# Kernel optimization log

Measured on AMD Instinct MI355X. Metric: run time of the kernel, lower is better.

The kernel has to match this reference:

```python
import jax, jax.numpy as jnp
import numpy as np

B, T, C, HS = 8, 2048, 1024, 128

def setup_inputs() -> dict:
    key = jax.random.key(0)
    kx, kq, kk, kv = jax.random.split(key, 4)
    x = jax.random.normal(kx, (B, T, C), dtype=jnp.float32)
    # torch Linear(C, HS, bias=False): y = x @ W^T with W [HS, C].
    # We store the transposed form [C, HS] and right-multiply (same math).
    scale = 1.0 / np.sqrt(C)  # torch default init scale-ish; exact init irrelevant for correctness
    Wq = jax.random.normal(kq, (C, HS), dtype=jnp.float32) * scale
    Wk = jax.random.normal(kk, (C, HS), dtype=jnp.float32) * scale
    Wv = jax.random.normal(kv, (C, HS), dtype=jnp.float32) * scale
    return {"x": x, "Wq": Wq, "Wk": Wk, "Wv": Wv}

def reference(x, Wq, Wk, Wv):
    Bx, Tx, Cx = x.shape
    q = x @ Wq  # [B, T, HS]
    k = x @ Wk
    v = x @ Wv
    # NOTE: original scales by C**-0.5 where C = n_embd (not head_size)
    wei = jnp.einsum('btd,bsd->bts', q, k) * (Cx ** -0.5)  # [B, T, T]
    causal = jnp.tril(jnp.ones((Tx, Tx), dtype=bool))
    wei = jnp.where(causal, wei, -jnp.inf)
    wei = jax.nn.softmax(wei, axis=-1)
    # dropout rate 0.0 (eval semantics) -> identity
    return jnp.einsum('bts,bsd->btd', wei, v)  # [B, T, HS]
```

## Files before the change

kernel.cpp:

```cpp
#include <hip/hip_runtime.h>
#include <hip/hip_bf16.h>
#include <stdint.h>

typedef float f32x4 __attribute__((ext_vector_type(4)));
typedef float f32x4v __attribute__((ext_vector_type(4)));
typedef short short8 __attribute__((ext_vector_type(8)));
typedef unsigned short u16;
typedef unsigned short u16x8 __attribute__((ext_vector_type(8)));
typedef unsigned short u16x4 __attribute__((ext_vector_type(4)));

#define MFMA16x16x32 __builtin_amdgcn_mfma_f32_16x16x32_bf16

__device__ __forceinline__ u16 f2bf(float f) {
    unsigned int u = __builtin_bit_cast(unsigned int, f);
    u += 0x7fffu + ((u >> 16) & 1u);
    return (u16)(u >> 16);
}

__device__ __forceinline__ void gload_lds16(const void* g, void* l) {
    __builtin_amdgcn_global_load_lds(
        (const __attribute__((address_space(1))) uint32_t*)g,
        (__attribute__((address_space(3))) uint32_t*)l, 16, 0, 0);
}

__device__ __forceinline__ int z_small(int na) {
    int za = (8 * na + 32) / 33;
    return za < 1 ? 1 : za;
}

__global__ void k_transpose_wf(const float* __restrict__ Wq, const float* __restrict__ Wk,
                               const float* __restrict__ Wv, u16* __restrict__ WTf) {
    int tid  = blockIdx.x * 256 + threadIdx.x;
    int f    = tid >> 6;
    int lane = tid & 63;
    int kt  = f / 48;
    int rem = f % 48;
    int ks  = rem / 24;
    int nc  = rem % 24;
    int col = nc * 16 + (lane & 15);
    int w   = col >> 7, n = col & 127;
    int k0  = kt * 64 + ks * 32 + (lane >> 4) * 8;
    const float* W = (w == 0) ? Wq : ((w == 1) ? Wk : Wv);
    u16x8 v;
#pragma unroll
    for (int j = 0; j < 8; ++j)
        v[j] = f2bf(W[(size_t)(k0 + j) * 128 + n]);
    *(u16x8*)(&WTf[(size_t)tid * 8]) = v;
}

__global__ __launch_bounds__(512) void k_qkv_gemm8(
    const float* __restrict__ x, const u16* __restrict__ WTf,
    u16* __restrict__ qb, u16* __restrict__ kb, u16* __restrict__ vT)
{
    __shared__ u16 abuf[2][64 * 64];
    __shared__ u16 bbuf[2][384 * 64];
    const int tid  = threadIdx.x;
    const int lane = tid & 63, wid = tid >> 6;
    const int wr = wid >> 2, wc = wid & 3;
    const int lrow = lane & 15, lk = lane >> 4;
    const int m0 = blockIdx.x * 64;

    const int arow = tid >> 3;
    const int aseg = tid & 7;
    const float* xsrc = x + (size_t)(m0 + arow) * 1024 + aseg * 8;

    f32x4 acc[2][6];
#pragma unroll
    for (int i = 0; i < 2; ++i)
#pragma unroll
        for (int j = 0; j < 6; ++j) acc[i][j] = (f32x4){0.f, 0.f, 0.f, 0.f};

#define LOADA(s0, s1, ktv)                                                     \
    s0 = *(const f32x4v*)(xsrc + (ktv) * 64);                                  \
    s1 = *(const f32x4v*)(xsrc + (ktv) * 64 + 4);

#define STOREA(buf, s0, s1)                                                    \
    {   u16x8 v;                                                               \
        v[0]=f2bf(s0[0]); v[1]=f2bf(s0[1]); v[2]=f2bf(s0[2]); v[3]=f2bf(s0[3]); \
        v[4]=f2bf(s1[0]); v[5]=f2bf(s1[1]); v[6]=f2bf(s1[2]); v[7]=f2bf(s1[3]); \
        *(u16x8*)(&buf[arow * 64 + ((aseg ^ (arow & 7)) << 3)]) = v; }

#define ISSUEB(buf, ktv)                                                       \
    {   const u16* bsrc = WTf + (size_t)(ktv) * 24576;                         \
        _Pragma("unroll") for (int i = 0; i < 6; ++i) {                        \
            int c = tid + i * 512;                                             \
            gload_lds16(bsrc + c * 8, &buf[c * 8]);                            \
        } }

#define COMPUTE(ab, bb)                                                        \
    _Pragma("unroll") for (int ks = 0; ks < 2; ++ks) {                         \
        short8 af[2];                                                          \
        _Pragma("unroll") for (int mf = 0; mf < 2; ++mf) {                     \
            int row = wr * 32 + mf * 16 + lrow;                                \
            int blk = (ks * 4 + lk) ^ (row & 7);                               \
            af[mf] = *(const short8*)(&ab[row * 64 + (blk << 3)]);             \
        }                                                                      \
        _Pragma("unroll") for (int nf = 0; nf < 6; ++nf) {                     \
            short8 bfr = *(const short8*)(&bb[(ks * 24 + wc * 6 + nf) * 512 + lane * 8]); \
            _Pragma("unroll") for (int mf = 0; mf < 2; ++mf)                   \
                acc[mf][nf] = MFMA16x16x32(af[mf], bfr, acc[mf][nf], 0, 0, 0); \
        } }

#define WAITBAR()                                                              \
    asm volatile("s_waitcnt vmcnt(2) lgkmcnt(0)\n\ts_barrier" ::: "memory");   \
    __builtin_amdgcn_sched_barrier(0);

    f32x4v a0A, a1A, a0B, a1B;
    LOADA(a0A, a1A, 0);
    LOADA(a0B, a1B, 1);
    STOREA(abuf[0], a0A, a1A);
    ISSUEB(bbuf[0], 0);
    LOADA(a0A, a1A, 2);
    WAITBAR();

    for (int kt = 0; kt < 16; kt += 2) {
        {
            const int ktn = (kt + 1 < 16) ? kt + 1 : 15;
            ISSUEB(bbuf[1], ktn);
            __builtin_amdgcn_sched_barrier(0);
            COMPUTE(abuf[0], bbuf[0]);
            STOREA(abuf[1], a0B, a1B);
            const int kp = (kt + 3 < 16) ? kt + 3 : 15;
            LOADA(a0B, a1B, kp);
            WAITBAR();
        }
        {
            const int ktn = (kt + 2 < 16) ? kt + 2 : 15;
            ISSUEB(bbuf[0], ktn);
            __builtin_amdgcn_sched_barrier(0);
            COMPUTE(abuf[1], bbuf[1]);
            STOREA(abuf[0], a0A, a1A);
            const int kp = (kt + 4 < 16) ? kt + 4 : 15;
            LOADA(a0A, a1A, kp);
            WAITBAR();
        }
    }
#undef LOADA
#undef STOREA
#undef ISSUEB
#undef COMPUTE
#undef WAITBAR

#pragma unroll
    for (int nf = 0; nf < 6; ++nf) {
        const int gc   = wc * 96 + nf * 16 + lrow;
        const int wsel = gc >> 7;
        const int col  = gc & 127;
#pragma unroll
        for (int mf = 0; mf < 2; ++mf) {
            const int row0 = m0 + wr * 32 + mf * 16 + lk * 4;
            if (wsel == 0) {
#pragma unroll
                for (int jj = 0; jj < 4; ++jj)
                    qb[(size_t)(row0 + jj) * 128 + col] = f2bf(acc[mf][nf][jj]);
            } else if (wsel == 1) {
#pragma unroll
                for (int jj = 0; jj < 4; ++jj)
                    kb[(size_t)(row0 + jj) * 128 + col] = f2bf(acc[mf][nf][jj]);
            } else {
                const int bb = row0 >> 11, t0 = row0 & 2047;
                u16x4 v;
#pragma unroll
                for (int jj = 0; jj < 4; ++jj) v[jj] = f2bf(acc[mf][nf][jj]);
                *(u16x4*)(&vT[((size_t)bb * 128 + col) * 2048 + t0]) = v;
            }
        }
    }
}

__global__ __launch_bounds__(256) void k_flash6(
    const u16* __restrict__ qb, const u16* __restrict__ kb, const u16* __restrict__ vT,
    float* __restrict__ po, float* __restrict__ pm, float* __restrict__ pl)
{
    __shared__ u16 k_lds[64 * 128];
    __shared__ u16 v_lds[128 * 64];
    __shared__ u16 p_lds[4 * 16 * 64];
    const int tid  = threadIdx.x;
    const int lane = tid & 63, wid = tid >> 6;
    const int lrow = lane & 15, lk = lane >> 4;
    const int bx = blockIdx.x;
    const int b  = bx & 7;
    const int p  = (bx >> 3) & 15;
    const int z  = bx >> 7;

    const int na = p + 1;
    const int za = z_small(na);
    int qt, n, k, Z;
    if (z < za) { qt = p;      n = na;     k = z;      Z = za;     }
    else        { qt = 31 - p; n = 32 - p; k = z - za; Z = 8 - za; }
    const int t0 = (k * n) / Z;
    const int t1 = ((k + 1) * n) / Z;

    const int qrow0 = qt * 64;
    short8 qf[4];
    {
        const u16* qp = qb + ((size_t)b * 2048 + qrow0 + wid * 16 + lrow) * 128;
#pragma unroll
        for (int ks = 0; ks < 4; ++ks) qf[ks] = *(const short8*)(qp + ks * 32 + lk * 8);
    }
    f32x4 of[8];
#pragma unroll
    for (int i = 0; i < 8; ++i) of[i] = (f32x4){0.f, 0.f, 0.f, 0.f};
    float mrun[4], lsum[4];
#pragma unroll
    for (int j = 0; j < 4; ++j) { mrun[j] = -1e30f; lsum[j] = 0.f; }

    const u16* kbase = kb + (size_t)b * 2048 * 128;
    const u16* vbase = vT + (size_t)b * 128 * 2048;
    u16* pw = p_lds + wid * (16 * 64);

    for (int t = t0; t < t1; ++t) {
        const int kv0 = t << 6;
        __syncthreads();
#pragma unroll
        for (int i = 0; i < 4; ++i) {
            int c = tid + i * 256;
            int row = c >> 4, blk = c & 15;
            gload_lds16(kbase + (size_t)(kv0 + row) * 128 + ((blk ^ (row & 7)) << 3),
                        &k_lds[c * 8]);
        }
#pragma unroll
        for (int i = 0; i < 4; ++i) {
            int c = tid + i * 256;
            int row = c >> 3, blk = c & 7;
            gload_lds16(vbase + (size_t)row * 2048 + kv0 + ((blk ^ (row & 7)) << 3),
                        &v_lds[c * 8]);
        }
        __syncthreads();

        f32x4 sf[4];
#pragma unroll
        for (int nf = 0; nf < 4; ++nf) sf[nf] = (f32x4){0.f, 0.f, 0.f, 0.f};
#pragma unroll
        for (int ks = 0; ks < 4; ++ks)
#pragma unroll
            for (int nf = 0; nf < 4; ++nf) {
                int row = nf * 16 + lrow;
                int blk = (ks * 4 + lk) ^ (row & 7);
                short8 bfr = *(const short8*)(&k_lds[row * 128 + (blk << 3)]);
                sf[nf] = MFMA16x16x32(qf[ks], bfr, sf[nf], 0, 0, 0);
            }

        const bool diag = (t == n - 1);
#pragma unroll
        for (int nf = 0; nf < 4; ++nf)
#pragma unroll
            for (int jj = 0; jj < 4; ++jj) {
                float s = sf[nf][jj] * 0.03125f;
                if (diag && (nf * 16 + lrow > wid * 16 + lk * 4 + jj)) s = -1e30f;
                sf[nf][jj] = s;
            }
        float mt[4];
#pragma unroll
        for (int jj = 0; jj < 4; ++jj)
            mt[jj] = fmaxf(fmaxf(sf[0][jj], sf[1][jj]), fmaxf(sf[2][jj], sf[3][jj]));
#pragma unroll
        for (int off = 1; off < 16; off <<= 1)
#pragma unroll
            for (int jj = 0; jj < 4; ++jj)
                mt[jj] = fmaxf(mt[jj], __shfl_xor(mt[jj], off));
        bool small = true;
#pragma unroll
        for (int jj = 0; jj < 4; ++jj) small = small && (mt[jj] <= mrun[jj] + 8.f);
        if (!__all(small)) {
#pragma unroll
            for (int jj = 0; jj < 4; ++jj) {
                float mnew = fmaxf(mrun[jj], mt[jj]);
                float sc   = __expf(mrun[jj] - mnew);
                mrun[jj]   = mnew;
                lsum[jj]  *= sc;
#pragma unroll
                for (int df = 0; df < 8; ++df) of[df][jj] *= sc;
            }
        }
        float rs[4] = {0.f, 0.f, 0.f, 0.f};
#pragma unroll
        for (int nf = 0; nf < 4; ++nf)
#pragma unroll
            for (int jj = 0; jj < 4; ++jj) {
                float e = __expf(sf[nf][jj] - mrun[jj]);
                sf[nf][jj] = e;
                rs[jj] += e;
            }
#pragma unroll
        for (int off = 1; off < 16; off <<= 1)
#pragma unroll
            for (int jj = 0; jj < 4; ++jj)
                rs[jj] += __shfl_xor(rs[jj], off);
#pragma unroll
        for (int jj = 0; jj < 4; ++jj) lsum[jj] += rs[jj];

#pragma unroll
        for (int nf = 0; nf < 4; ++nf)
#pragma unroll
            for (int jj = 0; jj < 4; ++jj) {
                int row = lk * 4 + jj;
                int col = nf * 16 + lrow;
                pw[row * 64 + (((col >> 3) ^ (row & 7)) << 3) + (col & 7)] = f2bf(sf[nf][jj]);
            }
        asm volatile("s_waitcnt lgkmcnt(0)" ::: "memory");
        __builtin_amdgcn_sched_barrier(0);
        short8 paf[2];
#pragma unroll
        for (int ks2 = 0; ks2 < 2; ++ks2) {
            int blk = (ks2 * 4 + lk) ^ (lrow & 7);
            paf[ks2] = *(const short8*)(&pw[lrow * 64 + (blk << 3)]);
        }
#pragma unroll
        for (int ks2 = 0; ks2 < 2; ++ks2)
#pragma unroll
            for (int df = 0; df < 8; ++df) {
                int row = df * 16 + lrow;
                int blk = (ks2 * 4 + lk) ^ (row & 7);
                short8 vf = *(const short8*)(&v_lds[row * 64 + (blk << 3)]);
                of[df] = MFMA16x16x32(paf[ks2], vf, of[df], 0, 0, 0);
            }
    }

    float* poslab = po + (size_t)bx * (64 * 128);
#pragma unroll
    for (int df = 0; df < 8; ++df)
#pragma unroll
        for (int jj = 0; jj < 4; ++jj)
            poslab[(size_t)(wid * 16 + lk * 4 + jj) * 128 + df * 16 + lrow] = of[df][jj];
    if (lrow == 0) {
#pragma unroll
        for (int jj = 0; jj < 4; ++jj) {
            pm[(size_t)bx * 64 + wid * 16 + lk * 4 + jj] = mrun[jj];
            pl[(size_t)bx * 64 + wid * 16 + lk * 4 + jj] = lsum[jj];
        }
    }
}

__global__ __launch_bounds__(256) void k_combine(
    const float* __restrict__ po, const float* __restrict__ pm, const float* __restrict__ pl,
    float* __restrict__ out)
{
    const int row  = blockIdx.x * 4 + (threadIdx.x >> 6);
    const int lane = threadIdx.x & 63;
    const int b  = row >> 11;
    const int t  = row & 2047;
    const int qt = t >> 6;
    const int r  = t & 63;

    const int p  = (qt < 16) ? qt : 31 - qt;
    const int za = z_small(p + 1);
    const int zlo = (qt < 16) ? 0 : za;
    const int zhi = (qt < 16) ? za : 8;

    float M = -1e30f;
    for (int z = zlo; z < zhi; ++z)
        M = fmaxf(M, pm[(size_t)(b + 8 * p + 128 * z) * 64 + r]);
    float den = 0.f, a0 = 0.f, a1 = 0.f;
    for (int z = zlo; z < zhi; ++z) {
        const int bxp = b + 8 * p + 128 * z;
        const float w = __expf(pm[(size_t)bxp * 64 + r] - M);
        den += w * pl[(size_t)bxp * 64 + r];
        const float* slab = po + ((size_t)bxp * 64 + r) * 128;
        a0 += w * slab[lane];
        a1 += w * slab[lane + 64];
    }
    const float inv = 1.f / den;
    out[(size_t)row * 128 + lane]      = a0 * inv;
    out[(size_t)row * 128 + lane + 64] = a1 * inv;
}

extern "C" void kernel_launch(void* const* d_in, const int* in_sizes, int n_in,
                              void* d_out, int out_size, void* d_ws, size_t ws_size,
                              hipStream_t stream) {
    const float* x  = (const float*)d_in[0];
    const float* Wq = (const float*)d_in[1];
    const float* Wk = (const float*)d_in[2];
    const float* Wv = (const float*)d_in[3];
    float* out = (float*)d_out;

    char* ws = (char*)d_ws;
    u16*   qb  = (u16*)(ws);
    u16*   kb  = (u16*)(ws + (size_t)4  * 1048576);
    u16*   vT  = (u16*)(ws + (size_t)8  * 1048576);
    u16*   WTf = (u16*)(ws + (size_t)12 * 1048576);
    float* po  = (float*)(ws + (size_t)13 * 1048576);
    float* pm  = (float*)(ws + (size_t)47 * 1048576);
    float* pl  = (float*)(ws + (size_t)48 * 1048576);

    k_transpose_wf<<<192, 256, 0, stream>>>(Wq, Wk, Wv, WTf);
    k_qkv_gemm8<<<256, 512, 0, stream>>>(x, WTf, qb, kb, vT);
    k_flash6<<<1024, 256, 0, stream>>>(qb, kb, vT, po, pm, pl);
    k_combine<<<4096, 256, 0, stream>>>(po, pm, pl, out);
}
```

Baseline: 78.86 us.

## Double-buffer K/V tiles in LDS and prefetch next tile during compute

The flash attention kernel now keeps two LDS buffers for K and V. It issues the async global-to-LDS loads for the next KV tile right after a single barrier, then computes on the current tile. This overlaps global memory latency with MFMA work and cuts the two barriers per iteration down to one. The cost is double the K/V LDS footprint, which may lower occupancy.

```diff
diff --git a/kernel.cpp b/kernel.cpp
--- a/kernel.cpp
+++ b/kernel.cpp
@@ -168,12 +168,12 @@
     }
 }
 
-__global__ __launch_bounds__(256) void k_flash6(
+__global__ __launch_bounds__(256) void k_flash7(
     const u16* __restrict__ qb, const u16* __restrict__ kb, const u16* __restrict__ vT,
     float* __restrict__ po, float* __restrict__ pm, float* __restrict__ pl)
 {
-    __shared__ u16 k_lds[64 * 128];
-    __shared__ u16 v_lds[128 * 64];
+    __shared__ u16 k_lds[2][64 * 128];
+    __shared__ u16 v_lds[2][128 * 64];
     __shared__ u16 p_lds[4 * 16 * 64];
     const int tid  = threadIdx.x;
     const int lane = tid & 63, wid = tid >> 6;
@@ -209,24 +209,29 @@
     const u16* vbase = vT + (size_t)b * 128 * 2048;
     u16* pw = p_lds + wid * (16 * 64);
 
+#define ISSUE_KV(c_, t_)                                                       \
+    {   const int kv0_ = (t_) << 6;                                            \
+        _Pragma("unroll") for (int i = 0; i < 4; ++i) {                        \
+            int ch = tid + i * 256;                                            \
+            int row = ch >> 4, blk = ch & 15;                                  \
+            gload_lds16(kbase + (size_t)(kv0_ + row) * 128 + ((blk ^ (row & 7)) << 3), \
+                        &k_lds[c_][ch * 8]);                                   \
+        }                                                                      \
+        _Pragma("unroll") for (int i = 0; i < 4; ++i) {                        \
+            int ch = tid + i * 256;                                            \
+            int row = ch >> 3, blk = ch & 7;                                   \
+            gload_lds16(vbase + (size_t)row * 2048 + kv0_ + ((blk ^ (row & 7)) << 3), \
+                        &v_lds[c_][ch * 8]);                                   \
+        }                                                                      \
+        __builtin_amdgcn_sched_barrier(0); }
+
+    ISSUE_KV(0, t0);
+    int c = 0;
+
     for (int t = t0; t < t1; ++t) {
-        const int kv0 = t << 6;
-        __syncthreads();
-#pragma unroll
-        for (int i = 0; i < 4; ++i) {
-            int c = tid + i * 256;
-            int row = c >> 4, blk = c & 15;
-            gload_lds16(kbase + (size_t)(kv0 + row) * 128 + ((blk ^ (row & 7)) << 3),
-                        &k_lds[c * 8]);
-        }
-#pragma unroll
-        for (int i = 0; i < 4; ++i) {
-            int c = tid + i * 256;
-            int row = c >> 3, blk = c & 7;
-            gload_lds16(vbase + (size_t)row * 2048 + kv0 + ((blk ^ (row & 7)) << 3),
-                        &v_lds[c * 8]);
-        }
-        __syncthreads();
+        asm volatile("s_waitcnt vmcnt(0) lgkmcnt(0)\n\ts_barrier" ::: "memory");
+        __builtin_amdgcn_sched_barrier(0);
+        if (t + 1 < t1) ISSUE_KV(c ^ 1, t + 1);
 
         f32x4 sf[4];
 #pragma unroll
@@ -237,7 +242,7 @@
             for (int nf = 0; nf < 4; ++nf) {
                 int row = nf * 16 + lrow;
                 int blk = (ks * 4 + lk) ^ (row & 7);
-                short8 bfr = *(const short8*)(&k_lds[row * 128 + (blk << 3)]);
+                short8 bfr = *(const short8*)(&k_lds[c][row * 128 + (blk << 3)]);
                 sf[nf] = MFMA16x16x32(qf[ks], bfr, sf[nf], 0, 0, 0);
             }
 
@@ -312,10 +317,12 @@
             for (int df = 0; df < 8; ++df) {
                 int row = df * 16 + lrow;
                 int blk = (ks2 * 4 + lk) ^ (row & 7);
-                short8 vf = *(const short8*)(&v_lds[row * 64 + (blk << 3)]);
+                short8 vf = *(const short8*)(&v_lds[c][row * 64 + (blk << 3)]);
                 of[df] = MFMA16x16x32(paf[ks2], vf, of[df], 0, 0, 0);
             }
-    }
+        c ^= 1;
+    }
+#undef ISSUE_KV
 
     float* poslab = po + (size_t)bx * (64 * 128);
 #pragma unroll
@@ -385,6 +392,6 @@
 
     k_transpose_wf<<<192, 256, 0, stream>>>(Wq, Wk, Wv, WTf);
     k_qkv_gemm8<<<256, 512, 0, stream>>>(x, WTf, qb, kb, vT);
-    k_flash6<<<1024, 256, 0, stream>>>(qb, kb, vT, po, pm, pl);
+    k_flash7<<<1024, 256, 0, stream>>>(qb, kb, vT, po, pm, pl);
     k_combine<<<4096, 256, 0, stream>>>(po, pm, pl, out);
 }
```

Result: faster. 76.67 us (-2.8%).

## Double KV tile to 128 in flash kernel and store partial outputs as bf16

Applied to the files above, without the earlier changes.

The flash-attention kernel now processes 128 keys per iteration instead of 64. This halves the number of loop trips, barriers and rescale checks, but needs larger LDS buffers and a general causal mask that checks absolute positions. The split-K work partition is recomputed for the new tile count. Partial output slabs are written as bf16 rather than fp32, which halves the traffic written by the flash kernel and read by the combine kernel, at some cost in precision. The larger LDS footprint and register use may reduce occupancy.

```diff
diff --git a/kernel.cpp b/kernel.cpp
--- a/kernel.cpp
+++ b/kernel.cpp
@@ -16,6 +16,10 @@
     u += 0x7fffu + ((u >> 16) & 1u);
     return (u16)(u >> 16);
 }
+__device__ __forceinline__ float bf2f(u16 v) {
+    unsigned int u = ((unsigned int)v) << 16;
+    return __builtin_bit_cast(float, u);
+}
 
 __device__ __forceinline__ void gload_lds16(const void* g, void* l) {
     __builtin_amdgcn_global_load_lds(
@@ -23,9 +27,11 @@
         (__attribute__((address_space(3))) uint32_t*)l, 16, 0, 0);
 }
 
-__device__ __forceinline__ int z_small(int na) {
-    int za = (8 * na + 32) / 33;
-    return za < 1 ? 1 : za;
+__device__ __forceinline__ int z_small128(int p) {
+    int na = (p + 2) >> 1;
+    int za = (8 * na + 16) / 17;
+    za = za < 1 ? 1 : za;
+    return za > 7 ? 7 : za;
 }
 
 __global__ void k_transpose_wf(const float* __restrict__ Wq, const float* __restrict__ Wk,
@@ -168,13 +174,13 @@
     }
 }
 
-__global__ __launch_bounds__(256) void k_flash6(
+__global__ __launch_bounds__(256) void k_flash9(
     const u16* __restrict__ qb, const u16* __restrict__ kb, const u16* __restrict__ vT,
-    float* __restrict__ po, float* __restrict__ pm, float* __restrict__ pl)
+    u16* __restrict__ po, float* __restrict__ pm, float* __restrict__ pl)
 {
-    __shared__ u16 k_lds[64 * 128];
-    __shared__ u16 v_lds[128 * 64];
-    __shared__ u16 p_lds[4 * 16 * 64];
+    __shared__ u16 k_lds[128 * 128];
+    __shared__ u16 v_lds[128 * 128];
+    __shared__ u16 p_lds[4 * 16 * 128];
     const int tid  = threadIdx.x;
     const int lane = tid & 63, wid = tid >> 6;
     const int lrow = lane & 15, lk = lane >> 4;
@@ -183,11 +189,10 @@
     const int p  = (bx >> 3) & 15;
     const int z  = bx >> 7;
 
-    const int na = p + 1;
-    const int za = z_small(na);
+    const int za = z_small128(p);
     int qt, n, k, Z;
-    if (z < za) { qt = p;      n = na;     k = z;      Z = za;     }
-    else        { qt = 31 - p; n = 32 - p; k = z - za; Z = 8 - za; }
+    if (z < za) { qt = p;      n = (p + 2) >> 1;  k = z;      Z = za;     }
+    else        { qt = 31 - p; n = (33 - p) >> 1; k = z - za; Z = 8 - za; }
     const int t0 = (k * n) / Z;
     const int t1 = ((k + 1) * n) / Z;
 
@@ -207,53 +212,59 @@
 
     const u16* kbase = kb + (size_t)b * 2048 * 128;
     const u16* vbase = vT + (size_t)b * 128 * 2048;
-    u16* pw = p_lds + wid * (16 * 64);
+    u16* pw = p_lds + wid * (16 * 128);
 
     for (int t = t0; t < t1; ++t) {
-        const int kv0 = t << 6;
+        const int kv0 = t << 7;
         __syncthreads();
 #pragma unroll
-        for (int i = 0; i < 4; ++i) {
-            int c = tid + i * 256;
-            int row = c >> 4, blk = c & 15;
+        for (int i = 0; i < 8; ++i) {
+            int ch = tid + i * 256;
+            int row = ch >> 4, blk = ch & 15;
             gload_lds16(kbase + (size_t)(kv0 + row) * 128 + ((blk ^ (row & 7)) << 3),
-                        &k_lds[c * 8]);
-        }
-#pragma unroll
-        for (int i = 0; i < 4; ++i) {
-            int c = tid + i * 256;
-            int row = c >> 3, blk = c & 7;
+                        &k_lds[ch * 8]);
+        }
+#pragma unroll
+        for (int i = 0; i < 8; ++i) {
+            int ch = tid + i * 256;
+            int row = ch >> 4, blk = ch & 15;
             gload_lds16(vbase + (size_t)row * 2048 + kv0 + ((blk ^ (row & 7)) << 3),
-                        &v_lds[c * 8]);
+                        &v_lds[ch * 8]);
         }
         __syncthreads();
 
-        f32x4 sf[4];
-#pragma unroll
-        for (int nf = 0; nf < 4; ++nf) sf[nf] = (f32x4){0.f, 0.f, 0.f, 0.f};
+        f32x4 sf[8];
+#pragma unroll
+        for (int nf = 0; nf < 8; ++nf) sf[nf] = (f32x4){0.f, 0.f, 0.f, 0.f};
 #pragma unroll
         for (int ks = 0; ks < 4; ++ks)
 #pragma unroll
-            for (int nf = 0; nf < 4; ++nf) {
+            for (int nf = 0; nf < 8; ++nf) {
                 int row = nf * 16 + lrow;
                 int blk = (ks * 4 + lk) ^ (row & 7);
                 short8 bfr = *(const short8*)(&k_lds[row * 128 + (blk << 3)]);
                 sf[nf] = MFMA16x16x32(qf[ks], bfr, sf[nf], 0, 0, 0);
             }
 
-        const bool diag = (t == n - 1);
-#pragma unroll
-        for (int nf = 0; nf < 4; ++nf)
+        const bool needmask = (kv0 + 127 > qrow0 + wid * 16);
+#pragma unroll
+        for (int nf = 0; nf < 8; ++nf)
 #pragma unroll
             for (int jj = 0; jj < 4; ++jj) {
                 float s = sf[nf][jj] * 0.03125f;
-                if (diag && (nf * 16 + lrow > wid * 16 + lk * 4 + jj)) s = -1e30f;
+                if (needmask &&
+                    (kv0 + nf * 16 + lrow > qrow0 + wid * 16 + lk * 4 + jj)) s = -1e30f;
                 sf[nf][jj] = s;
             }
         float mt[4];
 #pragma unroll
-        for (int jj = 0; jj < 4; ++jj)
-            mt[jj] = fmaxf(fmaxf(sf[0][jj], sf[1][jj]), fmaxf(sf[2][jj], sf[3][jj]));
+        for (int jj = 0; jj < 4; ++jj) {
+            float m01 = fmaxf(sf[0][jj], sf[1][jj]);
+            float m23 = fmaxf(sf[2][jj], sf[3][jj]);
+            float m45 = fmaxf(sf[4][jj], sf[5][jj]);
+            float m67 = fmaxf(sf[6][jj], sf[7][jj]);
+            mt[jj] = fmaxf(fmaxf(m01, m23), fmaxf(m45, m67));
+        }
 #pragma unroll
         for (int off = 1; off < 16; off <<= 1)
 #pragma unroll
@@ -275,7 +286,7 @@
         }
         float rs[4] = {0.f, 0.f, 0.f, 0.f};
 #pragma unroll
-        for (int nf = 0; nf < 4; ++nf)
+        for (int nf = 0; nf < 8; ++nf)
 #pragma unroll
             for (int jj = 0; jj < 4; ++jj) {
                 float e = __expf(sf[nf][jj] - mrun[jj]);
@@ -291,38 +302,38 @@
         for (int jj = 0; jj < 4; ++jj) lsum[jj] += rs[jj];
 
 #pragma unroll
-        for (int nf = 0; nf < 4; ++nf)
+        for (int nf = 0; nf < 8; ++nf)
 #pragma unroll
             for (int jj = 0; jj < 4; ++jj) {
                 int row = lk * 4 + jj;
                 int col = nf * 16 + lrow;
-                pw[row * 64 + (((col >> 3) ^ (row & 7)) << 3) + (col & 7)] = f2bf(sf[nf][jj]);
+                pw[row * 128 + (((col >> 3) ^ (row & 7)) << 3) + (col & 7)] = f2bf(sf[nf][jj]);
             }
         asm volatile("s_waitcnt lgkmcnt(0)" ::: "memory");
         __builtin_amdgcn_sched_barrier(0);
-        short8 paf[2];
-#pragma unroll
-        for (int ks2 = 0; ks2 < 2; ++ks2) {
+        short8 paf[4];
+#pragma unroll
+        for (int ks2 = 0; ks2 < 4; ++ks2) {
             int blk = (ks2 * 4 + lk) ^ (lrow & 7);
-            paf[ks2] = *(const short8*)(&pw[lrow * 64 + (blk << 3)]);
-        }
-#pragma unroll
-        for (int ks2 = 0; ks2 < 2; ++ks2)
+            paf[ks2] = *(const short8*)(&pw[lrow * 128 + (blk << 3)]);
+        }
+#pragma unroll
+        for (int ks2 = 0; ks2 < 4; ++ks2)
 #pragma unroll
             for (int df = 0; df < 8; ++df) {
                 int row = df * 16 + lrow;
                 int blk = (ks2 * 4 + lk) ^ (row & 7);
-                short8 vf = *(const short8*)(&v_lds[row * 64 + (blk << 3)]);
+                short8 vf = *(const short8*)(&v_lds[row * 128 + (blk << 3)]);
                 of[df] = MFMA16x16x32(paf[ks2], vf, of[df], 0, 0, 0);
             }
     }
 
-    float* poslab = po + (size_t)bx * (64 * 128);
+    u16* poslab = po + (size_t)bx * (64 * 128);
 #pragma unroll
     for (int df = 0; df < 8; ++df)
 #pragma unroll
         for (int jj = 0; jj < 4; ++jj)
-            poslab[(size_t)(wid * 16 + lk * 4 + jj) * 128 + df * 16 + lrow] = of[df][jj];
+            poslab[(size_t)(wid * 16 + lk * 4 + jj) * 128 + df * 16 + lrow] = f2bf(of[df][jj]);
     if (lrow == 0) {
 #pragma unroll
         for (int jj = 0; jj < 4; ++jj) {
@@ -333,7 +344,7 @@
 }
 
 __global__ __launch_bounds__(256) void k_combine(
-    const float* __restrict__ po, const float* __restrict__ pm, const float* __restrict__ pl,
+    const u16* __restrict__ po, const float* __restrict__ pm, const float* __restrict__ pl,
     float* __restrict__ out)
 {
     const int row  = blockIdx.x * 4 + (threadIdx.x >> 6);
@@ -344,7 +355,7 @@
     const int r  = t & 63;
 
     const int p  = (qt < 16) ? qt : 31 - qt;
-    const int za = z_small(p + 1);
+    const int za = z_small128(p);
     const int zlo = (qt < 16) ? 0 : za;
     const int zhi = (qt < 16) ? za : 8;
 
@@ -356,9 +367,9 @@
         const int bxp = b + 8 * p + 128 * z;
         const float w = __expf(pm[(size_t)bxp * 64 + r] - M);
         den += w * pl[(size_t)bxp * 64 + r];
-        const float* slab = po + ((size_t)bxp * 64 + r) * 128;
-        a0 += w * slab[lane];
-        a1 += w * slab[lane + 64];
+        const u16* slab = po + ((size_t)bxp * 64 + r) * 128;
+        a0 += w * bf2f(slab[lane]);
+        a1 += w * bf2f(slab[lane + 64]);
     }
     const float inv = 1.f / den;
     out[(size_t)row * 128 + lane]      = a0 * inv;
@@ -379,12 +390,12 @@
     u16*   kb  = (u16*)(ws + (size_t)4  * 1048576);
     u16*   vT  = (u16*)(ws + (size_t)8  * 1048576);
     u16*   WTf = (u16*)(ws + (size_t)12 * 1048576);
-    float* po  = (float*)(ws + (size_t)13 * 1048576);
+    u16*   po  = (u16*)(ws + (size_t)13 * 1048576);
     float* pm  = (float*)(ws + (size_t)47 * 1048576);
     float* pl  = (float*)(ws + (size_t)48 * 1048576);
 
     k_transpose_wf<<<192, 256, 0, stream>>>(Wq, Wk, Wv, WTf);
     k_qkv_gemm8<<<256, 512, 0, stream>>>(x, WTf, qb, kb, vT);
-    k_flash6<<<1024, 256, 0, stream>>>(qb, kb, vT, po, pm, pl);
+    k_flash9<<<1024, 256, 0, stream>>>(qb, kb, vT, po, pm, pl);
     k_combine<<<4096, 256, 0, stream>>>(po, pm, pl, out);
 }
```

Measured after the change: 74.68 us. -5.3%, faster.
